# Kernel tuning notes

Hardware: AMD Instinct MI355X
Metric: run time of the kernel (lower is better)

Reference implementation:

```python
import jax, jax.numpy as jnp
import numpy as np

BETA = 0.5
OT_ITER = 50
OT_K = 1
EPS = 1e-5


def _l2norm(x, eps=EPS):
    n = jnp.linalg.norm(x, axis=-1, keepdims=True)
    return x / jnp.maximum(n, eps)


def cost_matrix_cosine(x, y):
    # [B,M,D],[B,N,D] -> [B,M,N] cosine distance
    return 1.0 - jnp.einsum('bmd,bnd->bmn', _l2norm(x), _l2norm(y))


def ipot(C, x_len, x_pad, y_pad, y_len, joint_pad, beta, iteration, k):
    # C: [B,M,N] (already detached). Returns transport plan T: [B,N,M].
    b, m, n = C.shape
    jp_t = jnp.swapaxes(joint_pad, 1, 2)                      # [B,N,M]
    sigma = jnp.where(x_pad, 0.0, 1.0 / x_len[:, None])       # [B,M]
    sigma = sigma[:, :, None]                                 # [B,M,1]
    T = jnp.where(jp_t, 0.0, 1.0).astype(C.dtype)             # [B,N,M]
    A = jnp.where(jp_t, 0.0, jnp.exp(-jnp.swapaxes(C, 1, 2) / beta))
    x_mask = (x_pad.astype(C.dtype) * 1e4)[:, None, :]        # [B,1,M]
    y_mask = (y_pad.astype(C.dtype) * 1e4)[:, None, :]        # [B,1,N]
    xl = x_len[:, None, None]
    yl = y_len[:, None, None]

    def outer(carry, _):
        T, sigma = carry
        Q = A * T                                             # [B,N,M]

        def inner(sig, _):
            # sig: [B,M,1]
            delta = 1.0 / (yl * jnp.swapaxes(Q @ sig, 1, 2) + y_mask)   # [B,1,N]
            sig_new = 1.0 / (xl * (delta @ Q) + x_mask)                 # [B,1,M]
            return jnp.swapaxes(sig_new, 1, 2), delta

        sigma, deltas = jax.lax.scan(inner, sigma, None, length=k)
        delta = deltas[-1]                                    # [B,1,N]
        T_new = jnp.swapaxes(delta, 1, 2) * Q * jnp.swapaxes(sigma, 1, 2)
        return (T_new, sigma), None

    (T, _), _ = jax.lax.scan(outer, (T, sigma), None, length=iteration)
    return jnp.where(jp_t, 0.0, T)


def optimal_transport_dist(txt_emb, img_emb, txt_pad, img_pad,
                           beta=BETA, iteration=OT_ITER, k=OT_K):
    cost = cost_matrix_cosine(txt_emb, img_emb)               # [B,M,N]
    joint_pad = txt_pad[:, :, None] | img_pad[:, None, :]
    cost = jnp.where(joint_pad, 0.0, cost)
    txt_len = (txt_pad.shape[1] - txt_pad.sum(1)).astype(cost.dtype)
    img_len = (img_pad.shape[1] - img_pad.sum(1)).astype(cost.dtype)
    T = ipot(jax.lax.stop_gradient(cost), txt_len, txt_pad, img_pad,
             img_len, joint_pad, beta, iteration, k)
    T = jax.lax.stop_gradient(T)
    # trace(cost @ T)  == einsum over matching indices
    return jnp.einsum('bmn,bnm->b', cost, T)


def crf_llh(emissions, tags, mask, start_transitions, end_transitions, transitions):
    # emissions [T,B,K], tags [T,B] int, mask [T,B] bool (mask[0] all True)
    T, B, K = emissions.shape
    b_idx = jnp.arange(B)
    maskf = mask.astype(emissions.dtype)

    # numerator: gold path score
    score = start_transitions[tags[0]] + emissions[0, b_idx, tags[0]]
    trans_sc = transitions[tags[:-1], tags[1:]] * maskf[1:]              # [T-1,B]
    emit_sc = jnp.take_along_axis(emissions[1:], tags[1:][..., None], axis=-1)[..., 0] * maskf[1:]
    score = score + trans_sc.sum(0) + emit_sc.sum(0)
    seq_ends = mask.astype(jnp.int32).sum(0) - 1
    last_tags = tags[seq_ends, b_idx]
    numerator = score + end_transitions[last_tags]

    # denominator: forward algorithm (log-sum-exp recurrence)
    def step(s, inp):
        emis_t, mask_t = inp
        nxt = jax.nn.logsumexp(s[:, :, None] + transitions[None] + emis_t[:, None, :], axis=1)
        return jnp.where(mask_t[:, None], nxt, s), None

    init = start_transitions[None, :] + emissions[0]                     # [B,K]
    final, _ = jax.lax.scan(step, init, (emissions[1:], mask[1:]))
    denominator = jax.nn.logsumexp(final + end_transitions[None, :], axis=1)
    return numerator - denominator                                       # [B]


def setup_inputs() -> dict:
    key = jax.random.key(0)
    ks = jax.random.split(key, 10)
    T, B, K = 512, 64, 21
    M, N, D = 512, 512, 768

    emissions = jax.random.normal(ks[0], (T, B, K), dtype=jnp.float32)
    txt_emb = jax.random.normal(ks[1], (B, M, D), dtype=jnp.float32)
    img_emb = jax.random.normal(ks[2], (B, N, D), dtype=jnp.float32)

    start_transitions = jax.random.uniform(ks[3], (K,), minval=-0.1, maxval=0.1)
    end_transitions = jax.random.uniform(ks[4], (K,), minval=-0.1, maxval=0.1)
    transitions = jax.random.uniform(ks[5], (K, K), minval=-0.1, maxval=0.1)

    tags = jax.random.randint(ks[6], (T, B), 0, K)
    crf_len = jax.random.randint(ks[7], (B,), T // 2, T + 1)
    crf_mask = jnp.arange(T)[:, None] < crf_len[None, :]   # mask[0] all True
    txt_len = jax.random.randint(ks[8], (B,), M // 2, M + 1)
    txt_pad = jnp.arange(M)[None, :] >= txt_len[:, None]
    img_len = jax.random.randint(ks[9], (B,), N // 2, N + 1)
    img_pad = jnp.arange(N)[None, :] >= img_len[:, None]

    return {
        'emissions': emissions, 'txt_emb': txt_emb, 'img_emb': img_emb,
        'start_transitions': start_transitions, 'end_transitions': end_transitions,
        'transitions': transitions, 'tags': tags, 'crf_mask': crf_mask,
        'txt_pad': txt_pad, 'img_pad': img_pad,
    }


def reference(emissions, txt_emb, img_emb, start_transitions, end_transitions,
              transitions, tags, crf_mask, txt_pad, img_pad):
    llh = crf_llh(emissions, tags, crf_mask, start_transitions,
                  end_transitions, transitions)              # [B]
    ot = optimal_transport_dist(txt_emb, img_emb, txt_pad, img_pad)  # [B]
    loss = -llh.sum() + ot.sum()
    return loss
```

## Files before the change

kernel.cpp:

```cpp
#include <hip/hip_runtime.h>
#include <stdint.h>

typedef unsigned short u16;
typedef unsigned char u8;
typedef unsigned int u32;

#define LOG2E 1.4426950408889634f
#define LN2   0.6931471805599453f

__device__ __forceinline__ float exp2_(float x){ return __builtin_amdgcn_exp2f(x); }
__device__ __forceinline__ float log2_(float x){ return __builtin_amdgcn_logf(x); }
__device__ __forceinline__ float bflo(u32 u){ return __uint_as_float(u << 16); }
__device__ __forceinline__ float bfhi(u32 u){ return __uint_as_float(u & 0xffff0000u); }
__device__ __forceinline__ u16 f2bf(float f){
  u32 u = __float_as_uint(f);
  return (u16)((u + 0x7fffu + ((u >> 16) & 1u)) >> 16);
}
__device__ __forceinline__ u32 pkbf(float lo, float hi){
  u32 r; asm("v_cvt_pk_bf16_f32 %0, %1, %2" : "=v"(r) : "v"(lo), "v"(hi)); return r;
}
__device__ __forceinline__ int rdmask(const u8* p, int i, int st){ return (int)p[(size_t)i * st]; }

__global__ void k_detect(const u32* __restrict__ cmask, int* __restrict__ flags) {
  flags[0] = (cmask[0] == 0x01010101u) ? 1 : 4;
}

__global__ __launch_bounds__(256) void k_normalize(const float* __restrict__ txt,
                                                   const float* __restrict__ img,
                                                   u16* __restrict__ xh, u16* __restrict__ yh) {
  int row = blockIdx.x * 4 + (threadIdx.x >> 6);
  int l = threadIdx.x & 63;
  const float* src; u16* dst;
  if (row < 32768) { src = txt + (size_t)row * 768; dst = xh + (size_t)row * 768; }
  else { int r2 = row - 32768; src = img + (size_t)r2 * 768; dst = yh + (size_t)r2 * 768; }
  float v[12]; float ss = 0.f;
  #pragma unroll
  for (int s = 0; s < 12; ++s) { v[s] = src[l + (s << 6)]; ss = fmaf(v[s], v[s], ss); }
  #pragma unroll
  for (int off = 32; off; off >>= 1) ss += __shfl_xor(ss, off);
  float sc = 1.0f / fmaxf(sqrtf(ss), 1e-5f);
  #pragma unroll
  for (int s = 0; s < 12; ++s) dst[l + (s << 6)] = f2bf(v[s] * sc);
}

typedef __attribute__((ext_vector_type(8))) short short8;
typedef __attribute__((ext_vector_type(4))) float f32x4;

__global__ __launch_bounds__(256) void k_gemm_crf(const u16* __restrict__ xh, const u16* __restrict__ yh,
                                                  const u8* __restrict__ xpad, const u8* __restrict__ ypad,
                                                  const int* __restrict__ flags,
                                                  u16* __restrict__ Ct2,
                                                  const float* __restrict__ emis, const int* __restrict__ tags,
                                                  const u8* __restrict__ mask,
                                                  const float* __restrict__ startT, const float* __restrict__ endT,
                                                  const float* __restrict__ trans, float* __restrict__ llh) {
  __shared__ u16 As[128 * 64];
  __shared__ u16 Bs[128 * 64];
  __shared__ float tr[441];
  int st = flags[0];
  int bt = blockIdx.x;
  int tid = threadIdx.x;

  if (bt >= 1024) {
    int b = bt - 1024;
    for (int i = tid; i < 441; i += 256) tr[i] = trans[i];
    __syncthreads();
    if (tid >= 64) return;
    int k = tid;
    float accs = 0.f; int cnt = 0;
    for (int t = k; t < 512; t += 64) {
      int mt = rdmask(mask, (t << 6) + b, st);
      cnt += mt;
      int tg = tags[(t << 6) + b];
      if (t == 0) {
        accs += startT[tg] + emis[(size_t)b * 21 + tg];
      } else if (mt) {
        int tgp = tags[((t - 1) << 6) + b];
        accs += tr[tgp * 21 + tg] + emis[((size_t)((t << 6) + b)) * 21 + tg];
      }
    }
    #pragma unroll
    for (int off = 32; off; off >>= 1) { accs += __shfl_down(accs, off); cnt += __shfl_down(cnt, off); }
    float numer = 0.f;
    if (k == 0) {
      int last = tags[((cnt - 1) << 6) + b];
      numer = accs + endT[last];
    }
    int kc = (k < 21) ? k : 20;
    float s = startT[kc] + emis[(size_t)b * 21 + kc];
    for (int t = 1; t < 512; ++t) {
      float z[21];
      float zmax = -3.0e38f;
      #pragma unroll
      for (int j = 0; j < 21; ++j) {
        float sj = __shfl(s, j);
        z[j] = sj + tr[j * 21 + kc];
        zmax = fmaxf(zmax, z[j]);
      }
      float sum = 0.f;
      #pragma unroll
      for (int j = 0; j < 21; ++j) sum += exp2_((z[j] - zmax) * LOG2E);
      float ns = zmax + log2_(sum) * LN2 + emis[((size_t)((t << 6) + b)) * 21 + kc];
      s = rdmask(mask, (t << 6) + b, st) ? ns : s;
    }
    float f = (k < 21) ? (s + endT[kc]) : -3.0e38f;
    float m = f;
    #pragma unroll
    for (int off = 32; off; off >>= 1) m = fmaxf(m, __shfl_xor(m, off));
    float sum = (k < 21) ? exp2_((f - m) * LOG2E) : 0.f;
    #pragma unroll
    for (int off = 32; off; off >>= 1) sum += __shfl_xor(sum, off);
    float denom = m + log2_(sum) * LN2;
    if (k == 0) llh[b] = numer - denom;
    return;
  }

  int b = bt >> 4;
  int tile = bt & 15;
  int tn = tile >> 2, tm = tile & 3;
  const u16* Ab = yh + ((size_t)b * 512 + tn * 128) * 768;
  const u16* Bb = xh + ((size_t)b * 512 + tm * 128) * 768;
  int w = tid >> 6, l = tid & 63;
  int wr = (w >> 1) << 6, wc = (w & 1) << 6;
  f32x4 acc[4][4] = {};
  for (int k0 = 0; k0 < 768; k0 += 64) {
    #pragma unroll
    for (int q = 0; q < 4; ++q) {
      int slot = (q << 8) + tid;
      int row = slot >> 3, col = (slot & 7) << 3;
      uint4 va = *(const uint4*)(Ab + row * 768 + k0 + col);
      uint4 vb = *(const uint4*)(Bb + row * 768 + k0 + col);
      *(uint4*)((char*)As + slot * 16) = va;
      *(uint4*)((char*)Bs + slot * 16) = vb;
    }
    __syncthreads();
    #pragma unroll
    for (int kk = 0; kk < 64; kk += 32) {
      int cb = (kk + ((l >> 4) << 3)) * 2;
      short8 a[4], bb[4];
      #pragma unroll
      for (int i = 0; i < 4; ++i)
        a[i] = *(const short8*)((const char*)As + (wr + (i << 4) + (l & 15)) * 128 + cb);
      #pragma unroll
      for (int j = 0; j < 4; ++j)
        bb[j] = *(const short8*)((const char*)Bs + (wc + (j << 4) + (l & 15)) * 128 + cb);
      #pragma unroll
      for (int i = 0; i < 4; ++i)
        #pragma unroll
        for (int j = 0; j < 4; ++j)
          acc[i][j] = __builtin_amdgcn_mfma_f32_16x16x32_bf16(a[i], bb[j], acc[i][j], 0, 0, 0);
    }
    __syncthreads();
  }
  int n0 = (tn << 7) + wr, m0 = (tm << 7) + wc;
  #pragma unroll
  for (int i = 0; i < 4; ++i) {
    #pragma unroll
    for (int j = 0; j < 4; ++j) {
      int m = m0 + (j << 4) + (l & 15);
      int xpm = rdmask(xpad, b * 512 + m, st);
      #pragma unroll
      for (int r = 0; r < 4; ++r) {
        int n = n0 + (i << 4) + ((l >> 4) << 2) + r;
        float v = 2.8853901f * (1.0f - acc[i][j][r]);
        if (xpm | rdmask(ypad, b * 512 + n, st)) v = 30000.0f;
        Ct2[((size_t)(b * 512 + n) << 9) + m] = f2bf(v);
      }
    }
  }
}

__device__ __forceinline__ void batch_barrier(int* cnt, int target) {
  __syncthreads();
  if (threadIdx.x == 0) {
    __hip_atomic_fetch_add(cnt, 1, __ATOMIC_RELEASE, __HIP_MEMORY_SCOPE_AGENT);
    while (__hip_atomic_load(cnt, __ATOMIC_ACQUIRE, __HIP_MEMORY_SCOPE_AGENT) < target)
      __builtin_amdgcn_s_sleep(1);
  }
  __syncthreads();
}

__global__ __launch_bounds__(1024)
void k_ipot_pk(const u16* __restrict__ Ct2,
               const u8* __restrict__ xpad, const u8* __restrict__ ypad,
               const int* __restrict__ flags,
               int* __restrict__ gcount, float* __restrict__ c_part,
               float* __restrict__ fin_part,
               float* __restrict__ ot) {
  __shared__ __align__(16) u16  A_l[128 * 512];
  __shared__ __align__(16) float cpart[8][512];
  __shared__ __align__(16) float sig[512];
  __shared__ __align__(16) float xmk[512];
  __shared__ __align__(16) float ymk[512];
  __shared__ float redw[16];
  __shared__ int cnti[2];

  int bid = blockIdx.x;
  int b = bid & 63, p = bid >> 6;
  int tid = threadIdx.x;
  int w = tid >> 6, l = tid & 63;
  int st = flags[0];

  if (tid < 2) cnti[tid] = 0;
  __syncthreads();
  if (tid < 512) {
    int xp = rdmask(xpad, (b << 9) + tid, st) ? 1 : 0;
    int yp = rdmask(ypad, (b << 9) + tid, st) ? 1 : 0;
    xmk[tid] = xp ? 1e4f : 0.f;
    ymk[tid] = yp ? 1e4f : 0.f;
    atomicAdd(&cnti[0], 1 - xp);
    atomicAdd(&cnti[1], 1 - yp);
  }
  __syncthreads();
  float xl = (float)cnti[0], yl = (float)cnti[1];
  if (tid < 512) sig[tid] = (xmk[tid] > 0.f) ? 0.f : (1.0f / xl);

  const int base_n = p << 7;
  const int row0 = (w << 3);
  const u16* Cb = Ct2 + ((size_t)(b * 512 + base_n) << 9);
  int* cnt_b = gcount + (b << 6);
  float* cp_b = c_part + ((size_t)b << 12);

  u32 Tp[32];
  #pragma unroll
  for (int r = 0; r < 8; ++r) {
    const uint4 cv = *(const uint4*)(Cb + (size_t)(row0 + r) * 512 + (l << 3));
    uint4 av;
    av.x = pkbf(exp2_(-bflo(cv.x)), exp2_(-bfhi(cv.x)));
    av.y = pkbf(exp2_(-bflo(cv.y)), exp2_(-bfhi(cv.y)));
    av.z = pkbf(exp2_(-bflo(cv.z)), exp2_(-bfhi(cv.z)));
    av.w = pkbf(exp2_(-bflo(cv.w)), exp2_(-bfhi(cv.w)));
    *(uint4*)(A_l + (row0 + r) * 512 + (l << 3)) = av;
    Tp[r * 4 + 0] = 0x3F803F80u;
    Tp[r * 4 + 1] = 0x3F803F80u;
    Tp[r * 4 + 2] = 0x3F803F80u;
    Tp[r * 4 + 3] = 0x3F803F80u;
  }
  __syncthreads();

  for (int it = 1; it <= 50; ++it) {
    int par = it & 1;
    float dl[8];
    {
      float sg[8];
      const float4* ps = (const float4*)&sig[l << 3];
      float4 s0 = ps[0], s1 = ps[1];
      sg[0]=s0.x; sg[1]=s0.y; sg[2]=s0.z; sg[3]=s0.w;
      sg[4]=s1.x; sg[5]=s1.y; sg[6]=s1.z; sg[7]=s1.w;
      #pragma unroll
      for (int r = 0; r < 8; ++r) {
        const uint4 av = *(const uint4*)(A_l + (row0 + r) * 512 + (l << 3));
        float acc = 0.f;
        { u32 tw = Tp[r*4+0]; float q0 = bflo(av.x)*bflo(tw), q1 = bfhi(av.x)*bfhi(tw);
          Tp[r*4+0] = pkbf(q0,q1); acc = fmaf(q0,sg[0],acc); acc = fmaf(q1,sg[1],acc); }
        { u32 tw = Tp[r*4+1]; float q0 = bflo(av.y)*bflo(tw), q1 = bfhi(av.y)*bfhi(tw);
          Tp[r*4+1] = pkbf(q0,q1); acc = fmaf(q0,sg[2],acc); acc = fmaf(q1,sg[3],acc); }
        { u32 tw = Tp[r*4+2]; float q0 = bflo(av.z)*bflo(tw), q1 = bfhi(av.z)*bfhi(tw);
          Tp[r*4+2] = pkbf(q0,q1); acc = fmaf(q0,sg[4],acc); acc = fmaf(q1,sg[5],acc); }
        { u32 tw = Tp[r*4+3]; float q0 = bflo(av.w)*bflo(tw), q1 = bfhi(av.w)*bfhi(tw);
          Tp[r*4+3] = pkbf(q0,q1); acc = fmaf(q0,sg[6],acc); acc = fmaf(q1,sg[7],acc); }
        #pragma unroll
        for (int off = 32; off; off >>= 1) acc += __shfl_xor(acc, off);
        dl[r] = 1.0f / fmaf(yl, acc, ymk[base_n + row0 + r]);
      }
    }
    {
      float cp[8] = {0.f,0.f,0.f,0.f,0.f,0.f,0.f,0.f};
      #pragma unroll
      for (int r = 0; r < 8; ++r) {
        float d = dl[r];
        { u32 tw = Tp[r*4+0]; cp[0] = fmaf(bflo(tw),d,cp[0]); cp[1] = fmaf(bfhi(tw),d,cp[1]); }
        { u32 tw = Tp[r*4+1]; cp[2] = fmaf(bflo(tw),d,cp[2]); cp[3] = fmaf(bfhi(tw),d,cp[3]); }
        { u32 tw = Tp[r*4+2]; cp[4] = fmaf(bflo(tw),d,cp[4]); cp[5] = fmaf(bfhi(tw),d,cp[5]); }
        { u32 tw = Tp[r*4+3]; cp[6] = fmaf(bflo(tw),d,cp[6]); cp[7] = fmaf(bfhi(tw),d,cp[7]); }
      }
      if (w < 8) {
        float4* dst = (float4*)&cpart[w][l << 3];
        float4 v0, v1;
        v0.x=cp[0]; v0.y=cp[1]; v0.z=cp[2]; v0.w=cp[3];
        v1.x=cp[4]; v1.y=cp[5]; v1.z=cp[6]; v1.w=cp[7];
        dst[0] = v0; dst[1] = v1;
      }
      __syncthreads();
      if (w >= 8) {
        float4* dst = (float4*)&cpart[w - 8][l << 3];
        float4 v0 = dst[0], v1 = dst[1];
        v0.x+=cp[0]; v0.y+=cp[1]; v0.z+=cp[2]; v0.w+=cp[3];
        v1.x+=cp[4]; v1.y+=cp[5]; v1.z+=cp[6]; v1.w+=cp[7];
        dst[0] = v0; dst[1] = v1;
      }
      __syncthreads();
    }
    if (tid < 512) {
      float s = 0.f;
      #pragma unroll
      for (int k = 0; k < 8; ++k) s += cpart[k][tid];
      __hip_atomic_store(&cp_b[(par << 11) + (p << 9) + tid], s, __ATOMIC_RELAXED, __HIP_MEMORY_SCOPE_AGENT);
    }
    batch_barrier(&cnt_b[it - 1], 4);
    if (tid < 512) {
      const float* basep = cp_b + (par << 11);
      float s = __hip_atomic_load(&basep[tid], __ATOMIC_RELAXED, __HIP_MEMORY_SCOPE_AGENT);
      s += __hip_atomic_load(&basep[512 + tid], __ATOMIC_RELAXED, __HIP_MEMORY_SCOPE_AGENT);
      s += __hip_atomic_load(&basep[1024 + tid], __ATOMIC_RELAXED, __HIP_MEMORY_SCOPE_AGENT);
      s += __hip_atomic_load(&basep[1536 + tid], __ATOMIC_RELAXED, __HIP_MEMORY_SCOPE_AGENT);
      sig[tid] = 1.0f / fmaf(xl, s, xmk[tid]);
    }
    __syncthreads();
    {
      float sg[8];
      const float4* ps = (const float4*)&sig[l << 3];
      float4 s0 = ps[0], s1 = ps[1];
      sg[0]=s0.x; sg[1]=s0.y; sg[2]=s0.z; sg[3]=s0.w;
      sg[4]=s1.x; sg[5]=s1.y; sg[6]=s1.z; sg[7]=s1.w;
      #pragma unroll
      for (int r = 0; r < 8; ++r) {
        float d = dl[r];
        { u32 tw = Tp[r*4+0]; Tp[r*4+0] = pkbf(bflo(tw)*d*sg[0], bfhi(tw)*d*sg[1]); }
        { u32 tw = Tp[r*4+1]; Tp[r*4+1] = pkbf(bflo(tw)*d*sg[2], bfhi(tw)*d*sg[3]); }
        { u32 tw = Tp[r*4+2]; Tp[r*4+2] = pkbf(bflo(tw)*d*sg[4], bfhi(tw)*d*sg[5]); }
        { u32 tw = Tp[r*4+3]; Tp[r*4+3] = pkbf(bflo(tw)*d*sg[6], bfhi(tw)*d*sg[7]); }
      }
    }
  }

  float accT = 0.f;
  #pragma unroll
  for (int r = 0; r < 8; ++r) {
    const uint4 cv = *(const uint4*)(Cb + (size_t)(row0 + r) * 512 + (l << 3));
    { u32 tw = Tp[r*4+0]; accT = fmaf(bflo(cv.x), bflo(tw), accT); accT = fmaf(bfhi(cv.x), bfhi(tw), accT); }
    { u32 tw = Tp[r*4+1]; accT = fmaf(bflo(cv.y), bflo(tw), accT); accT = fmaf(bfhi(cv.y), bfhi(tw), accT); }
    { u32 tw = Tp[r*4+2]; accT = fmaf(bflo(cv.z), bflo(tw), accT); accT = fmaf(bfhi(cv.z), bfhi(tw), accT); }
    { u32 tw = Tp[r*4+3]; accT = fmaf(bflo(cv.w), bflo(tw), accT); accT = fmaf(bfhi(cv.w), bfhi(tw), accT); }
  }
  #pragma unroll
  for (int off = 32; off; off >>= 1) accT += __shfl_xor(accT, off);
  if (l == 0) redw[w] = accT;
  __syncthreads();
  if (tid == 0) {
    float s = 0.f;
    #pragma unroll
    for (int ww = 0; ww < 16; ++ww) s += redw[ww];
    __hip_atomic_store(&fin_part[(b << 2) + p], s, __ATOMIC_RELAXED, __HIP_MEMORY_SCOPE_AGENT);
  }
  batch_barrier(&cnt_b[50], 4);
  if (p == 0 && tid == 0) {
    float s = 0.f;
    #pragma unroll
    for (int pp = 0; pp < 4; ++pp)
      s += __hip_atomic_load(&fin_part[(b << 2) + pp], __ATOMIC_RELAXED, __HIP_MEMORY_SCOPE_AGENT);
    ot[b] = s * 0.34657359f;
  }
}

__global__ __launch_bounds__(64) void k_finalize(const float* __restrict__ llh, const float* __restrict__ ot,
                                                 float* __restrict__ out) {
  int l = threadIdx.x;
  float v = ot[l] - llh[l];
  #pragma unroll
  for (int off = 32; off; off >>= 1) v += __shfl_down(v, off);
  if (l == 0) out[0] = v;
}

extern "C" void kernel_launch(void* const* d_in, const int* in_sizes, int n_in,
                              void* d_out, int out_size, void* d_ws, size_t ws_size,
                              hipStream_t stream) {
  const float* emis  = (const float*)d_in[0];
  const float* txt   = (const float*)d_in[1];
  const float* img   = (const float*)d_in[2];
  const float* startT= (const float*)d_in[3];
  const float* endT  = (const float*)d_in[4];
  const float* trans = (const float*)d_in[5];
  const int*  tags   = (const int*)d_in[6];
  const u8* cmask = (const u8*)d_in[7];
  const u8* xpad  = (const u8*)d_in[8];
  const u8* ypad  = (const u8*)d_in[9];
  char* wsb = (char*)d_ws;
  u16* xh  = (u16*)wsb;
  u16* yh  = (u16*)(wsb + 50331648ll);
  u16* Ct2 = (u16*)(wsb + 100663296ll);
  float* ot    = (float*)(wsb + 134217728ll);
  float* llh   = ot + 64;
  int*  flags  = (int*)(llh + 64);
  int*  gcount = (int*)(wsb + 134218752ll);
  float* c_part= (float*)(wsb + 134235136ll);
  float* fin_part=(float*)(wsb + 135283712ll);
  float* out = (float*)d_out;

  hipMemsetAsync(gcount, 0, 64 * 64 * sizeof(int), stream);
  hipLaunchKernelGGL(k_detect, dim3(1), dim3(1), 0, stream, (const u32*)cmask, flags);
  hipLaunchKernelGGL(k_normalize, dim3(16384), dim3(256), 0, stream, txt, img, xh, yh);
  hipLaunchKernelGGL(k_gemm_crf, dim3(1088), dim3(256), 0, stream, xh, yh, xpad, ypad, flags, Ct2,
                     emis, tags, cmask, startT, endT, trans, llh);
  hipLaunchKernelGGL(k_ipot_pk, dim3(256), dim3(1024), 0, stream,
                     Ct2, xpad, ypad, flags, gcount, c_part, fin_part, ot);
  hipLaunchKernelGGL(k_finalize, dim3(1), dim3(64), 0, stream, llh, ot, out);
}
```

Measured before the change: 801.1 us.

## Store IPOT kernel matrix A in LDS as FP8 and shrink partial-sum buffer

The exp(-C/beta) matrix kept in shared memory is now packed as FP8 (four values per word) rather than bf16, halving LDS traffic and footprint. It is decoded with packed fp8->f32 conversions in the inner loop. The cross-wave column reduction buffer drops from 8 to 4 rows, at the cost of two extra block-wide barriers per iteration. FP8 storage lowers the precision of A and may shift the transport result.

```diff
diff --git a/kernel.cpp b/kernel.cpp
--- a/kernel.cpp
+++ b/kernel.cpp
@@ -7,6 +7,8 @@
 
 #define LOG2E 1.4426950408889634f
 #define LN2   0.6931471805599453f
+
+typedef __attribute__((ext_vector_type(2))) float f32x2;
 
 __device__ __forceinline__ float exp2_(float x){ return __builtin_amdgcn_exp2f(x); }
 __device__ __forceinline__ float log2_(float x){ return __builtin_amdgcn_logf(x); }
@@ -181,14 +183,14 @@
 }
 
 __global__ __launch_bounds__(1024)
-void k_ipot_pk(const u16* __restrict__ Ct2,
+void k_ipot_f8(const u16* __restrict__ Ct2,
                const u8* __restrict__ xpad, const u8* __restrict__ ypad,
                const int* __restrict__ flags,
                int* __restrict__ gcount, float* __restrict__ c_part,
                float* __restrict__ fin_part,
                float* __restrict__ ot) {
-  __shared__ __align__(16) u16  A_l[128 * 512];
-  __shared__ __align__(16) float cpart[8][512];
+  __shared__ __align__(16) u32  A_l[128 * 128];
+  __shared__ __align__(16) float cpart[4][512];
   __shared__ __align__(16) float sig[512];
   __shared__ __align__(16) float xmk[512];
   __shared__ __align__(16) float ymk[512];
@@ -225,12 +227,16 @@
   #pragma unroll
   for (int r = 0; r < 8; ++r) {
     const uint4 cv = *(const uint4*)(Cb + (size_t)(row0 + r) * 512 + (l << 3));
-    uint4 av;
-    av.x = pkbf(exp2_(-bflo(cv.x)), exp2_(-bfhi(cv.x)));
-    av.y = pkbf(exp2_(-bflo(cv.y)), exp2_(-bfhi(cv.y)));
-    av.z = pkbf(exp2_(-bflo(cv.z)), exp2_(-bfhi(cv.z)));
-    av.w = pkbf(exp2_(-bflo(cv.w)), exp2_(-bfhi(cv.w)));
-    *(uint4*)(A_l + (row0 + r) * 512 + (l << 3)) = av;
+    float a0 = exp2_(-bflo(cv.x)), a1 = exp2_(-bfhi(cv.x));
+    float a2 = exp2_(-bflo(cv.y)), a3 = exp2_(-bfhi(cv.y));
+    float a4 = exp2_(-bflo(cv.z)), a5 = exp2_(-bfhi(cv.z));
+    float a6 = exp2_(-bflo(cv.w)), a7 = exp2_(-bfhi(cv.w));
+    u32 w0 = (u32)__builtin_amdgcn_cvt_pk_fp8_f32(a0, a1, 0, false);
+    w0 = (u32)__builtin_amdgcn_cvt_pk_fp8_f32(a2, a3, (int)w0, true);
+    u32 w1 = (u32)__builtin_amdgcn_cvt_pk_fp8_f32(a4, a5, 0, false);
+    w1 = (u32)__builtin_amdgcn_cvt_pk_fp8_f32(a6, a7, (int)w1, true);
+    uint2 wv; wv.x = w0; wv.y = w1;
+    *(uint2*)(A_l + (row0 + r) * 128 + (l << 1)) = wv;
     Tp[r * 4 + 0] = 0x3F803F80u;
     Tp[r * 4 + 1] = 0x3F803F80u;
     Tp[r * 4 + 2] = 0x3F803F80u;
@@ -249,15 +255,19 @@
       sg[4]=s1.x; sg[5]=s1.y; sg[6]=s1.z; sg[7]=s1.w;
       #pragma unroll
       for (int r = 0; r < 8; ++r) {
-        const uint4 av = *(const uint4*)(A_l + (row0 + r) * 512 + (l << 3));
+        const uint2 av = *(const uint2*)(A_l + (row0 + r) * 128 + (l << 1));
+        f32x2 a01 = __builtin_amdgcn_cvt_pk_f32_fp8((int)av.x, false);
+        f32x2 a23 = __builtin_amdgcn_cvt_pk_f32_fp8((int)av.x, true);
+        f32x2 a45 = __builtin_amdgcn_cvt_pk_f32_fp8((int)av.y, false);
+        f32x2 a67 = __builtin_amdgcn_cvt_pk_f32_fp8((int)av.y, true);
         float acc = 0.f;
-        { u32 tw = Tp[r*4+0]; float q0 = bflo(av.x)*bflo(tw), q1 = bfhi(av.x)*bfhi(tw);
+        { u32 tw = Tp[r*4+0]; float q0 = a01.x*bflo(tw), q1 = a01.y*bfhi(tw);
           Tp[r*4+0] = pkbf(q0,q1); acc = fmaf(q0,sg[0],acc); acc = fmaf(q1,sg[1],acc); }
-        { u32 tw = Tp[r*4+1]; float q0 = bflo(av.y)*bflo(tw), q1 = bfhi(av.y)*bfhi(tw);
+        { u32 tw = Tp[r*4+1]; float q0 = a23.x*bflo(tw), q1 = a23.y*bfhi(tw);
           Tp[r*4+1] = pkbf(q0,q1); acc = fmaf(q0,sg[2],acc); acc = fmaf(q1,sg[3],acc); }
-        { u32 tw = Tp[r*4+2]; float q0 = bflo(av.z)*bflo(tw), q1 = bfhi(av.z)*bfhi(tw);
+        { u32 tw = Tp[r*4+2]; float q0 = a45.x*bflo(tw), q1 = a45.y*bfhi(tw);
           Tp[r*4+2] = pkbf(q0,q1); acc = fmaf(q0,sg[4],acc); acc = fmaf(q1,sg[5],acc); }
-        { u32 tw = Tp[r*4+3]; float q0 = bflo(av.w)*bflo(tw), q1 = bfhi(av.w)*bfhi(tw);
+        { u32 tw = Tp[r*4+3]; float q0 = a67.x*bflo(tw), q1 = a67.y*bfhi(tw);
           Tp[r*4+3] = pkbf(q0,q1); acc = fmaf(q0,sg[6],acc); acc = fmaf(q1,sg[7],acc); }
         #pragma unroll
         for (int off = 32; off; off >>= 1) acc += __shfl_xor(acc, off);
@@ -274,27 +284,36 @@
         { u32 tw = Tp[r*4+2]; cp[4] = fmaf(bflo(tw),d,cp[4]); cp[5] = fmaf(bfhi(tw),d,cp[5]); }
         { u32 tw = Tp[r*4+3]; cp[6] = fmaf(bflo(tw),d,cp[6]); cp[7] = fmaf(bfhi(tw),d,cp[7]); }
       }
-      if (w < 8) {
-        float4* dst = (float4*)&cpart[w][l << 3];
-        float4 v0, v1;
-        v0.x=cp[0]; v0.y=cp[1]; v0.z=cp[2]; v0.w=cp[3];
-        v1.x=cp[4]; v1.y=cp[5]; v1.z=cp[6]; v1.w=cp[7];
-        dst[0] = v0; dst[1] = v1;
-      }
+      float4 v0, v1;
+      v0.x=cp[0]; v0.y=cp[1]; v0.z=cp[2]; v0.w=cp[3];
+      v1.x=cp[4]; v1.y=cp[5]; v1.z=cp[6]; v1.w=cp[7];
+      float4* dst = (float4*)&cpart[w & 3][l << 3];
+      if (w < 4) { dst[0] = v0; dst[1] = v1; }
       __syncthreads();
-      if (w >= 8) {
-        float4* dst = (float4*)&cpart[w - 8][l << 3];
-        float4 v0 = dst[0], v1 = dst[1];
-        v0.x+=cp[0]; v0.y+=cp[1]; v0.z+=cp[2]; v0.w+=cp[3];
-        v1.x+=cp[4]; v1.y+=cp[5]; v1.z+=cp[6]; v1.w+=cp[7];
-        dst[0] = v0; dst[1] = v1;
+      if (w >= 4 && w < 8) {
+        float4 o0 = dst[0], o1 = dst[1];
+        o0.x+=v0.x; o0.y+=v0.y; o0.z+=v0.z; o0.w+=v0.w;
+        o1.x+=v1.x; o1.y+=v1.y; o1.z+=v1.z; o1.w+=v1.w;
+        dst[0] = o0; dst[1] = o1;
       }
       __syncthreads();
+      if (w >= 8 && w < 12) {
+        float4 o0 = dst[0], o1 = dst[1];
+        o0.x+=v0.x; o0.y+=v0.y; o0.z+=v0.z; o0.w+=v0.w;
+        o1.x+=v1.x; o1.y+=v1.y; o1.z+=v1.z; o1.w+=v1.w;
+        dst[0] = o0; dst[1] = o1;
+      }
+      __syncthreads();
+      if (w >= 12) {
+        float4 o0 = dst[0], o1 = dst[1];
+        o0.x+=v0.x; o0.y+=v0.y; o0.z+=v0.z; o0.w+=v0.w;
+        o1.x+=v1.x; o1.y+=v1.y; o1.z+=v1.z; o1.w+=v1.w;
+        dst[0] = o0; dst[1] = o1;
+      }
+      __syncthreads();
     }
     if (tid < 512) {
-      float s = 0.f;
-      #pragma unroll
-      for (int k = 0; k < 8; ++k) s += cpart[k][tid];
+      float s = cpart[0][tid] + cpart[1][tid] + cpart[2][tid] + cpart[3][tid];
       __hip_atomic_store(&cp_b[(par << 11) + (p << 9) + tid], s, __ATOMIC_RELAXED, __HIP_MEMORY_SCOPE_AGENT);
     }
     batch_barrier(&cnt_b[it - 1], 4);
@@ -392,7 +411,7 @@
   hipLaunchKernelGGL(k_normalize, dim3(16384), dim3(256), 0, stream, txt, img, xh, yh);
   hipLaunchKernelGGL(k_gemm_crf, dim3(1088), dim3(256), 0, stream, xh, yh, xpad, ypad, flags, Ct2,
                      emis, tags, cmask, startT, endT, trans, llh);
-  hipLaunchKernelGGL(k_ipot_pk, dim3(256), dim3(1024), 0, stream,
+  hipLaunchKernelGGL(k_ipot_f8, dim3(256), dim3(1024), 0, stream,
                      Ct2, xpad, ypad, flags, gcount, c_part, fin_part, ot);
   hipLaunchKernelGGL(k_finalize, dim3(1), dim3(64), 0, stream, llh, ot, out);
 }
```

Measured after the change: 803.4 us. No clear change (+0.3%).
